# Performance work log

Measured on AMD Instinct MI355X. Metric: run time of the kernel, lower is better.

Reference implementation:

```python
import jax, jax.numpy as jnp
import numpy as np


def get_mgrid(slen):
    # replicates bliss get_mgrid: np.mgrid / offset, dstack((y, x)), scaled by (slen-1)/slen
    offset = (slen - 1) / 2.0
    c = (np.arange(slen, dtype=np.float32) - offset) / offset  # in [-1, 1]
    g = np.zeros((slen, slen, 2), dtype=np.float32)
    g[:, :, 0] = c[None, :]  # x-coordinate (varies along width, axis 1)
    g[:, :, 1] = c[:, None]  # y-coordinate (varies along height, axis 0)
    return jnp.asarray(g * (slen - 1) / slen)


def grid_sample_bilinear_zeros(img, grid):
    # img: [N, C, H, W]; grid: [N, Ho, Wo, 2] with (x, y) normalized coords.
    # F.grid_sample(mode='bilinear', padding_mode='zeros', align_corners=True)
    N, C, H, W = img.shape
    ix = (grid[..., 0] + 1.0) * 0.5 * (W - 1)  # [N, Ho, Wo]
    iy = (grid[..., 1] + 1.0) * 0.5 * (H - 1)
    ix0 = jnp.floor(ix)
    iy0 = jnp.floor(iy)
    wx1 = ix - ix0
    wy1 = iy - iy0
    wx0 = 1.0 - wx1
    wy0 = 1.0 - wy1

    def corner(iy_f, ix_f, w):
        valid = ((ix_f >= 0) & (ix_f <= W - 1) & (iy_f >= 0) & (iy_f <= H - 1)).astype(img.dtype)
        ixc = jnp.clip(ix_f, 0, W - 1).astype(jnp.int32)
        iyc = jnp.clip(iy_f, 0, H - 1).astype(jnp.int32)

        def gather_one(im, iy1, ix1, m):
            # im: [C, H, W]; iy1/ix1/m: [Ho, Wo] -> [C, Ho, Wo]
            return im[:, iy1, ix1] * m[None]

        vals = jax.vmap(gather_one)(img, iyc, ixc, valid)  # [N, C, Ho, Wo]
        return vals * w[:, None, :, :]

    return (
        corner(iy0, ix0, wy0 * wx0)
        + corner(iy0, ix0 + 1.0, wy0 * wx1)
        + corner(iy0 + 1.0, ix0, wy1 * wx0)
        + corner(iy0 + 1.0, ix0 + 1.0, wy1 * wx1)
    )


def setup_inputs() -> dict:
    key = jax.random.key(0)
    k1, k2 = jax.random.split(key)
    n_ptiles, max_src, n_bands = 1024, 4, 5
    tile_slen, ptile_slen = 4, 52
    locs = jax.random.uniform(k1, (n_ptiles, max_src, 2), dtype=jnp.float32)
    sources = jax.random.normal(k2, (n_ptiles, max_src, n_bands, ptile_slen, ptile_slen), dtype=jnp.float32)
    return {"locs": locs, "sources": sources, "tile_slen": tile_slen, "ptile_slen": ptile_slen}


def reference(locs, sources, tile_slen, ptile_slen):
    n_ptiles, max_src, n_bands, s, _ = sources.shape
    # location transform (from _render_one_source)
    padding = (ptile_slen - tile_slen) / 2.0
    l = locs * (tile_slen / ptile_slen) + padding / ptile_slen
    l = (l - 0.5) * 2.0
    l_sw = l[..., ::-1]  # index_select with swap=[1,0]: (y,x) -> (x,y)
    mgrid = get_mgrid(ptile_slen)  # [P, P, 2]
    # grid for all sources at once: [n_ptiles, max_src, P, P, 2]
    grid = mgrid[None, None] - l_sw[:, :, None, None, :]
    imgs = sources.reshape(n_ptiles * max_src, n_bands, s, s)
    grid = grid.reshape(n_ptiles * max_src, ptile_slen, ptile_slen, 2)
    sampled = grid_sample_bilinear_zeros(imgs, grid)
    # accumulate over sources (the python loop + ptile += in the original)
    return sampled.reshape(n_ptiles, max_src, n_bands, ptile_slen, ptile_slen).sum(axis=1)
```

## Files before the change

kernel.cpp:

```cpp
#include <hip/hip_runtime.h>

constexpr int NP = 1024;
constexpr int MS = 4;
constexpr int NB = 5;
constexpr int SL = 52;
constexpr int SS = SL * SL;
constexpr int NTHR = 256;
constexpr int NJ = 11;
constexpr int TAIL = SS - (NJ - 1) * NTHR;
constexpr int NCH = SS / 4;
constexpr int FPAD = 4;
constexpr int PY = 2;
constexpr int BUFF = FPAD + (SL + 2 * PY) * SL + FPAD;
constexpr int INT0 = FPAD + PY * SL;

__device__ __forceinline__ void gload_lds16(const float* g, float* l) {
    __builtin_amdgcn_global_load_lds(
        (const __attribute__((address_space(1))) void*)g,
        (__attribute__((address_space(3))) void*)l,
        16, 0, 0);
}

__global__ __launch_bounds__(NTHR) void tile_render_kernel(
    const float* __restrict__ locs,
    const float* __restrict__ sources,
    float* __restrict__ out)
{
    __shared__ __align__(16) float smem[2 * BUFF];

    const int blk = blockIdx.x;
    const int p = blk / NB;
    const int b = blk - p * NB;
    const int tid = threadIdx.x;

    for (int i = 4 * tid; i < 2 * BUFF; i += 4 * NTHR)
        *reinterpret_cast<float4*>(smem + i) = make_float4(0.f, 0.f, 0.f, 0.f);

    const float A = 25.5f / 26.0f;
    float bx[MS], by[MS];
    #pragma unroll
    for (int s = 0; s < MS; ++s) {
        float loc0 = locs[(p * MS + s) * 2 + 0];
        float loc1 = locs[(p * MS + s) * 2 + 1];
        float l0 = (loc0 * (4.0f / 52.0f) + (24.0f / 52.0f) - 0.5f) * 2.0f;
        float l1 = (loc1 * (4.0f / 52.0f) + (24.0f / 52.0f) - 0.5f) * 2.0f;
        bx[s] = (1.0f - l1) * 25.5f - 25.5f * 25.5f / 26.0f;
        by[s] = (1.0f - l0) * 25.5f - 25.5f * 25.5f / 26.0f;
    }

    float fx[NJ], fy[NJ];
    #pragma unroll
    for (int j = 0; j < NJ; ++j) {
        int pix = tid + j * NTHR;
        if (pix >= SS) pix = 0;
        int y = pix / SL;
        fx[j] = (float)(pix - y * SL);
        fy[j] = (float)y;
    }

    const float* gsrc = sources + ((size_t)p * MS * NB + b) * SS;
    auto stage = [&](float* buf, int s) {
        const float* g = gsrc + (size_t)s * (NB * SS);
        float* dst = buf + INT0;
        gload_lds16(g + 4 * tid,          dst + 4 * tid);
        gload_lds16(g + 4 * (tid + NTHR), dst + 4 * (tid + NTHR));
        if (tid < NCH - 2 * NTHR)
            gload_lds16(g + 4 * (tid + 2 * NTHR), dst + 4 * (tid + 2 * NTHR));
    };

    float acc[NJ];
    #pragma unroll
    for (int j = 0; j < NJ; ++j) acc[j] = 0.0f;

    __syncthreads();
    stage(smem, 0);

    #pragma unroll
    for (int s = 0; s < MS; ++s) {
        __syncthreads();
        if (s < MS - 1) stage(smem + ((s + 1) & 1) * BUFF, s + 1);

        const float* cur = smem + (s & 1) * BUFF;
        const float bxs = bx[s], bys = by[s];
        #pragma unroll
        for (int j = 0; j < NJ; ++j) {
            float ix = fmaf(fx[j], A, bxs);
            float iy = fmaf(fy[j], A, bys);
            float ixf = floorf(ix);
            float iyf = floorf(iy);
            float wx = ix - ixf;
            float wy = iy - iyf;
            int xi = (int)ixf;
            int yi = (int)iyf;
            float wx0 = 1.0f - wx;
            float wxa = ((unsigned)xi       <= 51u) ? wx0 : 0.0f;
            float wxb = ((unsigned)(xi + 1) <= 51u) ? wx  : 0.0f;
            int xc = min(max(xi, -1), SL - 1);
            const float* q = cur + (yi * SL + (xc + INT0));
            float v00 = q[0],  v01 = q[1];
            float v10 = q[SL], v11 = q[SL + 1];
            float h0 = fmaf(v01, wxb, v00 * wxa);
            float h1 = fmaf(v11, wxb, v10 * wxa);
            acc[j] = fmaf(wy, h1 - h0, h0 + acc[j]);
        }
    }

    float* outp = out + ((size_t)p * NB + b) * SS;
    #pragma unroll
    for (int j = 0; j < NJ; ++j) {
        int pix = tid + j * NTHR;
        if (j < NJ - 1 || tid < TAIL) outp[pix] = acc[j];
    }
}

extern "C" void kernel_launch(void* const* d_in, const int* in_sizes, int n_in,
                              void* d_out, int out_size, void* d_ws, size_t ws_size,
                              hipStream_t stream) {
    const float* locs = (const float*)d_in[0];
    const float* sources = (const float*)d_in[1];
    float* out = (float*)d_out;
    dim3 grid(NP * NB);
    dim3 block(NTHR);
    hipLaunchKernelGGL(tile_render_kernel, grid, block, 0, stream,
                       locs, sources, out);
}
```

Measured before the change: 48.89 us.

## Map threads to column-by-row-group layout and hoist per-column x interpolation

New measurement: 87.41 us. +78.8%, slower.

```diff
diff --git a/kernel.cpp b/kernel.cpp
--- a/kernel.cpp
+++ b/kernel.cpp
@@ -6,13 +6,13 @@
 constexpr int SL = 52;
 constexpr int SS = SL * SL;
 constexpr int NTHR = 256;
-constexpr int NJ = 11;
-constexpr int TAIL = SS - (NJ - 1) * NTHR;
+constexpr int NROW = 13;
 constexpr int NCH = SS / 4;
 constexpr int FPAD = 4;
 constexpr int PY = 2;
 constexpr int BUFF = FPAD + (SL + 2 * PY) * SL + FPAD;
 constexpr int INT0 = FPAD + PY * SL;
+constexpr int PADF = 2 * (FPAD + PY * SL);
 
 __device__ __forceinline__ void gload_lds16(const float* g, float* l) {
     __builtin_amdgcn_global_load_lds(
@@ -33,8 +33,11 @@
     const int b = blk - p * NB;
     const int tid = threadIdx.x;
 
-    for (int i = 4 * tid; i < 2 * BUFF; i += 4 * NTHR)
-        *reinterpret_cast<float4*>(smem + i) = make_float4(0.f, 0.f, 0.f, 0.f);
+    if (tid < PADF) {
+        int off = (tid < INT0) ? tid : (SS + tid);
+        smem[off] = 0.0f;
+        smem[BUFF + off] = 0.0f;
+    }
 
     const float A = 25.5f / 26.0f;
     float bx[MS], by[MS];
@@ -48,15 +51,9 @@
         by[s] = (1.0f - l0) * 25.5f - 25.5f * 25.5f / 26.0f;
     }
 
-    float fx[NJ], fy[NJ];
-    #pragma unroll
-    for (int j = 0; j < NJ; ++j) {
-        int pix = tid + j * NTHR;
-        if (pix >= SS) pix = 0;
-        int y = pix / SL;
-        fx[j] = (float)(pix - y * SL);
-        fy[j] = (float)y;
-    }
+    const int x = tid & 63;
+    const int yg = tid >> 6;
+    const float fxv = (float)x;
 
     const float* gsrc = sources + ((size_t)p * MS * NB + b) * SS;
     auto stage = [&](float* buf, int s) {
@@ -68,11 +65,10 @@
             gload_lds16(g + 4 * (tid + 2 * NTHR), dst + 4 * (tid + 2 * NTHR));
     };
 
-    float acc[NJ];
+    float acc[NROW];
     #pragma unroll
-    for (int j = 0; j < NJ; ++j) acc[j] = 0.0f;
+    for (int k = 0; k < NROW; ++k) acc[k] = 0.0f;
 
-    __syncthreads();
     stage(smem, 0);
 
     #pragma unroll
@@ -81,35 +77,36 @@
         if (s < MS - 1) stage(smem + ((s + 1) & 1) * BUFF, s + 1);
 
         const float* cur = smem + (s & 1) * BUFF;
-        const float bxs = bx[s], bys = by[s];
+        float ix = fmaf(fxv, A, bx[s]);
+        float ixf = floorf(ix);
+        float wx = ix - ixf;
+        int xi = (int)ixf;
+        float wxa = ((unsigned)xi       <= 51u) ? (1.0f - wx) : 0.0f;
+        float wxb = ((unsigned)(xi + 1) <= 51u) ? wx          : 0.0f;
+        int xc = min(max(xi, -1), SL - 1);
+        const float* colbase = cur + (xc + INT0);
+        const float bys = by[s];
         #pragma unroll
-        for (int j = 0; j < NJ; ++j) {
-            float ix = fmaf(fx[j], A, bxs);
-            float iy = fmaf(fy[j], A, bys);
-            float ixf = floorf(ix);
+        for (int k = 0; k < NROW; ++k) {
+            float fyv = (float)(yg + 4 * k);
+            float iy = fmaf(fyv, A, bys);
             float iyf = floorf(iy);
-            float wx = ix - ixf;
             float wy = iy - iyf;
-            int xi = (int)ixf;
             int yi = (int)iyf;
-            float wx0 = 1.0f - wx;
-            float wxa = ((unsigned)xi       <= 51u) ? wx0 : 0.0f;
-            float wxb = ((unsigned)(xi + 1) <= 51u) ? wx  : 0.0f;
-            int xc = min(max(xi, -1), SL - 1);
-            const float* q = cur + (yi * SL + (xc + INT0));
+            const float* q = colbase + yi * SL;
             float v00 = q[0],  v01 = q[1];
             float v10 = q[SL], v11 = q[SL + 1];
             float h0 = fmaf(v01, wxb, v00 * wxa);
             float h1 = fmaf(v11, wxb, v10 * wxa);
-            acc[j] = fmaf(wy, h1 - h0, h0 + acc[j]);
+            acc[k] = fmaf(wy, h1 - h0, h0 + acc[k]);
         }
     }
 
-    float* outp = out + ((size_t)p * NB + b) * SS;
-    #pragma unroll
-    for (int j = 0; j < NJ; ++j) {
-        int pix = tid + j * NTHR;
-        if (j < NJ - 1 || tid < TAIL) outp[pix] = acc[j];
+    if (x < SL) {
+        float* outp = out + ((size_t)p * NB + b) * SS + x;
+        #pragma unroll
+        for (int k = 0; k < NROW; ++k)
+            outp[(yg + 4 * k) * SL] = acc[k];
     }
 }
 
```

## Split each ptile into row bands and stage only needed source rows

Applied to the files above, without the earlier changes.

Result: slower. 152.9 us (+212.7%).

```diff
diff --git a/kernel.cpp b/kernel.cpp
--- a/kernel.cpp
+++ b/kernel.cpp
@@ -6,13 +6,13 @@
 constexpr int SL = 52;
 constexpr int SS = SL * SL;
 constexpr int NTHR = 256;
-constexpr int NJ = 11;
-constexpr int TAIL = SS - (NJ - 1) * NTHR;
-constexpr int NCH = SS / 4;
+constexpr int RPB = 13;
+constexpr int PXB = RPB * SL;
+constexpr int NJ  = 3;
+constexpr int SROWS = 14;
 constexpr int FPAD = 4;
-constexpr int PY = 2;
-constexpr int BUFF = FPAD + (SL + 2 * PY) * SL + FPAD;
-constexpr int INT0 = FPAD + PY * SL;
+constexpr int BUFF = FPAD + SROWS * SL + FPAD;
+constexpr int NPH = MS * NB;
 
 __device__ __forceinline__ void gload_lds16(const float* g, float* l) {
     __builtin_amdgcn_global_load_lds(
@@ -29,15 +29,13 @@
     __shared__ __align__(16) float smem[2 * BUFF];
 
     const int blk = blockIdx.x;
-    const int p = blk / NB;
-    const int b = blk - p * NB;
+    const int p = blk >> 2;
+    const int h = blk & 3;
     const int tid = threadIdx.x;
 
-    for (int i = 4 * tid; i < 2 * BUFF; i += 4 * NTHR)
-        *reinterpret_cast<float4*>(smem + i) = make_float4(0.f, 0.f, 0.f, 0.f);
-
     const float A = 25.5f / 26.0f;
-    float bx[MS], by[MS];
+    float bx[MS], byr[MS];
+    int gsa[MS], topa[MS], cnta[MS];
     #pragma unroll
     for (int s = 0; s < MS; ++s) {
         float loc0 = locs[(p * MS + s) * 2 + 0];
@@ -45,71 +43,98 @@
         float l0 = (loc0 * (4.0f / 52.0f) + (24.0f / 52.0f) - 0.5f) * 2.0f;
         float l1 = (loc1 * (4.0f / 52.0f) + (24.0f / 52.0f) - 0.5f) * 2.0f;
         bx[s] = (1.0f - l1) * 25.5f - 25.5f * 25.5f / 26.0f;
-        by[s] = (1.0f - l0) * 25.5f - 25.5f * 25.5f / 26.0f;
+        float by = (1.0f - l0) * 25.5f - 25.5f * 25.5f / 26.0f;
+        float byh = fmaf((float)(RPB * h), A, by);
+        int r0 = (int)floorf(byh);
+        byr[s] = byh - (float)r0;
+        int gs = max(r0, 0);
+        int ge = min(r0 + SROWS - 1, SL - 1);
+        gsa[s] = gs;
+        topa[s] = gs - r0;
+        cnta[s] = ge - gs + 1;
     }
 
-    float fx[NJ], fy[NJ];
+    int xs_[NJ], obase[NJ];
+    float yls[NJ];
     #pragma unroll
     for (int j = 0; j < NJ; ++j) {
-        int pix = tid + j * NTHR;
-        if (pix >= SS) pix = 0;
-        int y = pix / SL;
-        fx[j] = (float)(pix - y * SL);
-        fy[j] = (float)y;
+        int px = tid + j * NTHR;
+        int pv = (px < PXB) ? px : 0;
+        int yl = pv / SL;
+        int x = pv - yl * SL;
+        xs_[j] = x;
+        yls[j] = (float)yl;
+        obase[j] = (RPB * h + yl) * SL + x;
     }
 
-    const float* gsrc = sources + ((size_t)p * MS * NB + b) * SS;
-    auto stage = [&](float* buf, int s) {
-        const float* g = gsrc + (size_t)s * (NB * SS);
-        float* dst = buf + INT0;
-        gload_lds16(g + 4 * tid,          dst + 4 * tid);
-        gload_lds16(g + 4 * (tid + NTHR), dst + 4 * (tid + NTHR));
-        if (tid < NCH - 2 * NTHR)
-            gload_lds16(g + 4 * (tid + 2 * NTHR), dst + 4 * (tid + 2 * NTHR));
+    const float* gtile = sources + (size_t)p * (MS * NB * SS);
+
+    auto stage = [&](int s2, int b2, float* slot) {
+        int top = topa[s2], cnt = cnta[s2];
+        if (tid < top * SL) slot[FPAD + tid] = 0.0f;
+        int bo = FPAD + (top + cnt) * SL;
+        if (tid < (FPAD + SROWS * SL - bo)) slot[bo + tid] = 0.0f;
+        if (tid < FPAD) { slot[tid] = 0.0f; slot[FPAD + SROWS * SL + tid] = 0.0f; }
+        if (tid < cnt * (SL / 4)) {
+            const float* g = gtile + ((size_t)s2 * NB + b2) * SS + gsa[s2] * SL + 4 * tid;
+            gload_lds16(g, slot + FPAD + top * SL + 4 * tid);
+        }
     };
 
-    float acc[NJ];
+    float acc[NJ][NB];
     #pragma unroll
-    for (int j = 0; j < NJ; ++j) acc[j] = 0.0f;
+    for (int j = 0; j < NJ; ++j)
+        #pragma unroll
+        for (int b = 0; b < NB; ++b) acc[j][b] = 0.0f;
 
-    __syncthreads();
-    stage(smem, 0);
+    stage(0, 0, smem);
 
     #pragma unroll
     for (int s = 0; s < MS; ++s) {
-        __syncthreads();
-        if (s < MS - 1) stage(smem + ((s + 1) & 1) * BUFF, s + 1);
-
-        const float* cur = smem + (s & 1) * BUFF;
-        const float bxs = bx[s], bys = by[s];
+        int adr[NJ];
+        float wxa[NJ], wxb[NJ], wwy[NJ];
         #pragma unroll
         for (int j = 0; j < NJ; ++j) {
-            float ix = fmaf(fx[j], A, bxs);
-            float iy = fmaf(fy[j], A, bys);
+            float ix = fmaf((float)xs_[j], A, bx[s]);
             float ixf = floorf(ix);
+            float wx = ix - ixf;
+            int xi = (int)ixf;
+            wxa[j] = ((unsigned)xi       <= 51u) ? (1.0f - wx) : 0.0f;
+            wxb[j] = ((unsigned)(xi + 1) <= 51u) ? wx          : 0.0f;
+            int xc = min(max(xi, -1), SL - 1);
+            float iy = fmaf(yls[j], A, byr[s]);
             float iyf = floorf(iy);
-            float wx = ix - ixf;
-            float wy = iy - iyf;
-            int xi = (int)ixf;
-            int yi = (int)iyf;
-            float wx0 = 1.0f - wx;
-            float wxa = ((unsigned)xi       <= 51u) ? wx0 : 0.0f;
-            float wxb = ((unsigned)(xi + 1) <= 51u) ? wx  : 0.0f;
-            int xc = min(max(xi, -1), SL - 1);
-            const float* q = cur + (yi * SL + (xc + INT0));
-            float v00 = q[0],  v01 = q[1];
-            float v10 = q[SL], v11 = q[SL + 1];
-            float h0 = fmaf(v01, wxb, v00 * wxa);
-            float h1 = fmaf(v11, wxb, v10 * wxa);
-            acc[j] = fmaf(wy, h1 - h0, h0 + acc[j]);
+            wwy[j] = iy - iyf;
+            int k = (int)iyf;
+            adr[j] = k * SL + xc + FPAD;
+        }
+        #pragma unroll
+        for (int b = 0; b < NB; ++b) {
+            const int i = NB * s + b;
+            __syncthreads();
+            if (i + 1 < NPH)
+                stage((i + 1) / NB, (i + 1) % NB, smem + ((i + 1) & 1) * BUFF);
+            const float* cur = smem + (i & 1) * BUFF;
+            #pragma unroll
+            for (int j = 0; j < NJ; ++j) {
+                const float* q = cur + adr[j];
+                float v00 = q[0],  v01 = q[1];
+                float v10 = q[SL], v11 = q[SL + 1];
+                float h0 = fmaf(v01, wxb[j], v00 * wxa[j]);
+                float h1 = fmaf(v11, wxb[j], v10 * wxa[j]);
+                acc[j][b] = fmaf(wwy[j], h1 - h0, h0 + acc[j][b]);
+            }
         }
     }
 
-    float* outp = out + ((size_t)p * NB + b) * SS;
+    float* op = out + (size_t)p * (NB * SS);
     #pragma unroll
     for (int j = 0; j < NJ; ++j) {
-        int pix = tid + j * NTHR;
-        if (j < NJ - 1 || tid < TAIL) outp[pix] = acc[j];
+        if (tid + j * NTHR < PXB) {
+            #pragma unroll
+            for (int b = 0; b < NB; ++b)
+                __builtin_nontemporal_store(acc[j][b], op + b * SS + obase[j]);
+        }
     }
 }
 
@@ -119,7 +144,7 @@
     const float* locs = (const float*)d_in[0];
     const float* sources = (const float*)d_in[1];
     float* out = (float*)d_out;
-    dim3 grid(NP * NB);
+    dim3 grid(NP * 4);
     dim3 block(NTHR);
     hipLaunchKernelGGL(tile_render_kernel, grid, block, 0, stream,
                        locs, sources, out);
```

## Compute vertically adjacent output pixel pairs per thread to share LDS row loads

Applied to the files above, without the earlier changes.

Measured after the change: 48.26 us. About the same (-1.3%).

```diff
diff --git a/kernel.cpp b/kernel.cpp
--- a/kernel.cpp
+++ b/kernel.cpp
@@ -6,8 +6,9 @@
 constexpr int SL = 52;
 constexpr int SS = SL * SL;
 constexpr int NTHR = 256;
-constexpr int NJ = 11;
-constexpr int TAIL = SS - (NJ - 1) * NTHR;
+constexpr int NPAIR = SS / 2;
+constexpr int NJ = 6;
+constexpr int PTAIL = NPAIR - (NJ - 1) * NTHR;
 constexpr int NCH = SS / 4;
 constexpr int FPAD = 4;
 constexpr int PY = 2;
@@ -48,14 +49,14 @@
         by[s] = (1.0f - l0) * 25.5f - 25.5f * 25.5f / 26.0f;
     }
 
-    float fx[NJ], fy[NJ];
+    float fxv[NJ], fyv[NJ];
     #pragma unroll
     for (int j = 0; j < NJ; ++j) {
-        int pix = tid + j * NTHR;
-        if (pix >= SS) pix = 0;
-        int y = pix / SL;
-        fx[j] = (float)(pix - y * SL);
-        fy[j] = (float)y;
+        int pp = tid + j * NTHR;
+        if (pp >= NPAIR) pp = 0;
+        int yp = pp / SL;
+        fxv[j] = (float)(pp - yp * SL);
+        fyv[j] = (float)(2 * yp);
     }
 
     const float* gsrc = sources + ((size_t)p * MS * NB + b) * SS;
@@ -68,9 +69,9 @@
             gload_lds16(g + 4 * (tid + 2 * NTHR), dst + 4 * (tid + 2 * NTHR));
     };
 
-    float acc[NJ];
+    float acc0[NJ], acc1[NJ];
     #pragma unroll
-    for (int j = 0; j < NJ; ++j) acc[j] = 0.0f;
+    for (int j = 0; j < NJ; ++j) { acc0[j] = 0.0f; acc1[j] = 0.0f; }
 
     __syncthreads();
     stage(smem, 0);
@@ -84,32 +85,45 @@
         const float bxs = bx[s], bys = by[s];
         #pragma unroll
         for (int j = 0; j < NJ; ++j) {
-            float ix = fmaf(fx[j], A, bxs);
-            float iy = fmaf(fy[j], A, bys);
+            float ix = fmaf(fxv[j], A, bxs);
             float ixf = floorf(ix);
-            float iyf = floorf(iy);
             float wx = ix - ixf;
-            float wy = iy - iyf;
             int xi = (int)ixf;
-            int yi = (int)iyf;
-            float wx0 = 1.0f - wx;
-            float wxa = ((unsigned)xi       <= 51u) ? wx0 : 0.0f;
-            float wxb = ((unsigned)(xi + 1) <= 51u) ? wx  : 0.0f;
+            float wxa = ((unsigned)xi       <= 51u) ? (1.0f - wx) : 0.0f;
+            float wxb = ((unsigned)(xi + 1) <= 51u) ? wx          : 0.0f;
             int xc = min(max(xi, -1), SL - 1);
-            const float* q = cur + (yi * SL + (xc + INT0));
-            float v00 = q[0],  v01 = q[1];
-            float v10 = q[SL], v11 = q[SL + 1];
-            float h0 = fmaf(v01, wxb, v00 * wxa);
-            float h1 = fmaf(v11, wxb, v10 * wxa);
-            acc[j] = fmaf(wy, h1 - h0, h0 + acc[j]);
+            float iy1 = fmaf(fyv[j],        A, bys);
+            float iy2 = fmaf(fyv[j] + 1.0f, A, bys);
+            float f1 = floorf(iy1), f2 = floorf(iy2);
+            float wy1 = iy1 - f1,   wy2 = iy2 - f2;
+            int r  = (int)f1;
+            int r2 = (int)f2;
+            int base = min(r, SL - 1);
+            bool o1 = (r != base);
+            bool o2 = (r2 - base >= 1);
+            const float* q = cur + (base * SL + (xc + INT0));
+            float a0 = q[0],       a1 = q[1];
+            float b0 = q[SL],      b1 = q[SL + 1];
+            float c0 = q[2 * SL],  c1 = q[2 * SL + 1];
+            float h0 = fmaf(a1, wxb, a0 * wxa);
+            float h1 = fmaf(b1, wxb, b0 * wxa);
+            float h2 = fmaf(c1, wxb, c0 * wxa);
+            float p1lo = o1 ? h1 : h0, p1hi = o1 ? h2 : h1;
+            float p2lo = o2 ? h1 : h0, p2hi = o2 ? h2 : h1;
+            acc0[j] = fmaf(wy1, p1hi - p1lo, p1lo + acc0[j]);
+            acc1[j] = fmaf(wy2, p2hi - p2lo, p2lo + acc1[j]);
         }
     }
 
     float* outp = out + ((size_t)p * NB + b) * SS;
     #pragma unroll
     for (int j = 0; j < NJ; ++j) {
-        int pix = tid + j * NTHR;
-        if (j < NJ - 1 || tid < TAIL) outp[pix] = acc[j];
+        if (j < NJ - 1 || tid < PTAIL) {
+            int x = (int)fxv[j];
+            int o = (int)fyv[j] * SL + x;
+            __builtin_nontemporal_store(acc0[j], outp + o);
+            __builtin_nontemporal_store(acc1[j], outp + o + SL);
+        }
     }
 }
 
```
